# Performance work log

Measured on AMD Instinct MI355X. Metric: run time of the kernel, lower is better.

Reference implementation:

```python
import jax, jax.numpy as jnp
import numpy as np

N, L, D = 32, 4096, 768
H = 12
DH = D // H
MLP_DIM = 4 * D


def setup_inputs() -> dict:
    key = jax.random.key(0)
    ks = jax.random.split(key, 12)
    xavier = jax.nn.initializers.xavier_uniform()
    inp = {
        "x": jax.random.normal(ks[0], (N, L, D), jnp.float32),
        "probe": xavier(ks[1], (1, 1, D), jnp.float32),
        # MHA projections (flax DenseGeneral layout: (d, h, dh) / out (h, dh, d))
        "wq": xavier(ks[2], (D, H, DH), jnp.float32),
        "bq": jnp.zeros((H, DH), jnp.float32),
        "wk": xavier(ks[3], (D, H, DH), jnp.float32),
        "bk": jnp.zeros((H, DH), jnp.float32),
        "wv": xavier(ks[4], (D, H, DH), jnp.float32),
        "bv": jnp.zeros((H, DH), jnp.float32),
        "wo": xavier(ks[5], (H, DH, D), jnp.float32),
        "bo": jnp.zeros((D,), jnp.float32),
        # LayerNorm
        "ln_scale": jnp.ones((D,), jnp.float32),
        "ln_bias": jnp.zeros((D,), jnp.float32),
        # MLP block
        "w1": xavier(ks[6], (D, MLP_DIM), jnp.float32),
        "b1": jax.random.normal(ks[7], (MLP_DIM,), jnp.float32) * 1e-6,
        "w2": xavier(ks[8], (MLP_DIM, D), jnp.float32),
        "b2": jax.random.normal(ks[9], (D,), jnp.float32) * 1e-6,
    }
    return inp


def _layernorm(x, scale, bias, eps=1e-6):
    mu = jnp.mean(x, axis=-1, keepdims=True)
    var = jnp.mean(jnp.square(x - mu), axis=-1, keepdims=True)
    return (x - mu) * jax.lax.rsqrt(var + eps) * scale + bias


def reference(x, probe, wq, bq, wk, bk, wv, bv, wo, bo,
              ln_scale, ln_bias, w1, b1, w2, b2):
    n, l, d = x.shape
    q_in = jnp.broadcast_to(probe, (n, 1, d))          # tile probe over batch
    q = jnp.einsum('nqd,dhe->nqhe', q_in, wq) + bq     # [n,1,h,dh]
    k = jnp.einsum('nld,dhe->nlhe', x, wk) + bk        # [n,l,h,dh]
    v = jnp.einsum('nld,dhe->nlhe', x, wv) + bv
    q = q / jnp.sqrt(jnp.asarray(DH, q.dtype))
    logits = jnp.einsum('nqhe,nlhe->nhql', q, k)       # [n,h,1,l]
    attn = jax.nn.softmax(logits, axis=-1)
    o = jnp.einsum('nhql,nlhe->nqhe', attn, v)         # [n,1,h,dh]
    xa = jnp.einsum('nqhe,hed->nqd', o, wo) + bo       # attention output [n,1,d]
    y = _layernorm(xa, ln_scale, ln_bias)
    mlp = jnp.dot(jax.nn.gelu(jnp.dot(y, w1) + b1), w2) + b2
    out = xa + mlp
    return out[:, 0]                                   # [n,d]
```

## Files before the change

### kernel.cpp

```cpp
#include <hip/hip_runtime.h>
#include <math.h>

#define N_B 32
#define L_S 4096
#define D_M 768
#define H_N 12
#define NCH 16

#define ZO_QH    0
#define ZO_O     1024
#define ZO_XA    25600
#define ZO_H1P   50176
#define ZO_MACC  148480
#define ZERO_N   173056
#define NZ_QK    173056
#define NZ_QB    182272
#define NZ_MLC   182336
#define NZ_SLC   188480
#define NZ_SCL   194624
#define NZ_XBP   200768
#define NZ_Y     4919360

__global__ __launch_bounds__(256) void qh_kernel(
    const float* __restrict__ probe, const float* __restrict__ wq,
    const float* __restrict__ bq, float* __restrict__ qh) {
    int i = blockIdx.x * 256 + threadIdx.x;
    int d0 = blockIdx.y * 48;
    float acc = 0.f;
    for (int dd = 0; dd < 48; ++dd)
        acc += probe[d0 + dd] * wq[(size_t)(d0 + dd) * 768 + i];
    acc *= 0.125f;
    if (blockIdx.y == 0) acc += 0.125f * bq[i];
    atomicAdd(&qh[i], acc);
}

__global__ __launch_bounds__(256) void qk_kernel(
    const float* __restrict__ qh, const float* __restrict__ wk,
    const float* __restrict__ bk, float* __restrict__ qk,
    float* __restrict__ qb) {
    int h = blockIdx.x, dt = blockIdx.y, t = threadIdx.x;
    int d = dt * 256 + t;
    const float4* wk4 = (const float4*)(wk + (size_t)d * 768 + h * 64);
    const float4* qh4 = (const float4*)(qh + h * 64);
    float acc = 0.f;
    #pragma unroll
    for (int e4 = 0; e4 < 16; ++e4) {
        float4 w = wk4[e4], q = qh4[e4];
        acc += w.x * q.x + w.y * q.y + w.z * q.z + w.w * q.w;
    }
    qk[h * 768 + d] = acc;
    if (dt == 0 && t < 64) {
        float v = qh[h * 64 + t] * bk[h * 64 + t];
        #pragma unroll
        for (int off = 32; off > 0; off >>= 1) v += __shfl_xor(v, off);
        if (t == 0) qb[h] = v;
    }
}

__global__ __launch_bounds__(256) void attn_fused(
    const float* __restrict__ x, const float* __restrict__ qk,
    const float* __restrict__ qb, float* __restrict__ xbp,
    float* __restrict__ mlc, float* __restrict__ slc) {
    __shared__ __align__(16) float qk_s[12 * 772];
    __shared__ __align__(16) float xs[2 * 4 * 772];
    __shared__ float lg_s[64], w_s[64], qb_s[16], ms_s[16], ss_s[16], sc_s[16];
    int lc = blockIdx.x, n = blockIdx.y, t = threadIdx.x;
    int lane = t & 63, w = t >> 6;
    size_t xbase = ((size_t)n * 4096 + lc * 256) * 768;

    for (int i = t; i < 12 * 192; i += 256) {
        int hh = i / 192, c = i % 192;
        ((float4*)&qk_s[hh * 772])[c] = ((const float4*)qk)[i];
    }
    if (t < 12) { qb_s[t] = qb[t]; ms_s[t] = -1e30f; ss_s[t] = 0.f; }
    {
        const float4* s0 = (const float4*)(x + xbase);
        for (int j = t; j < 768; j += 256) {
            float4 v = s0[j];
            *((float4*)&xs[(j / 192) * 772 + (j % 192) * 4]) = v;
        }
    }
    float acc[12][3];
    #pragma unroll
    for (int h = 0; h < 12; ++h) { acc[h][0] = 0.f; acc[h][1] = 0.f; acc[h][2] = 0.f; }
    int q = t & 3, rh = t >> 2, h1 = rh % 12, r1 = t / 48;
    int d0 = t * 3;
    __syncthreads();

    int p = 0;
    for (int it = 0; it < 64; ++it) {
        if (w == 3 && it + 1 < 64) {
            const float4* src = (const float4*)(x + xbase + (size_t)(it + 1) * 3072);
            #pragma unroll
            for (int j = 0; j < 12; ++j) {
                int f = lane + 64 * j;
                float4 v = src[f];
                *((float4*)&xs[(p ^ 1) * 3088 + (f / 192) * 772 + (f % 192) * 4]) = v;
            }
        }
        if (t < 192) {
            const float4* xr = (const float4*)&xs[p * 3088 + r1 * 772];
            const float4* kr = (const float4*)&qk_s[h1 * 772];
            float a = 0.f;
            #pragma unroll 8
            for (int s = 0; s < 48; ++s) {
                int idx = s * 4 + q;
                float4 xv = xr[idx], kv = kr[idx];
                a += xv.x * kv.x + xv.y * kv.y + xv.z * kv.z + xv.w * kv.w;
            }
            a += __shfl_xor(a, 1);
            a += __shfl_xor(a, 2);
            if (q == 0) lg_s[r1 * 16 + h1] = a + qb_s[h1];
        }
        __syncthreads();
        if (t < 12) {
            float l0 = lg_s[0 * 16 + t], l1 = lg_s[1 * 16 + t];
            float l2 = lg_s[2 * 16 + t], l3 = lg_s[3 * 16 + t];
            float mt = fmaxf(fmaxf(l0, l1), fmaxf(l2, l3));
            float mo = ms_s[t];
            float mn = fmaxf(mo, mt);
            float sc = __expf(mo - mn);
            float e0 = __expf(l0 - mn), e1 = __expf(l1 - mn);
            float e2 = __expf(l2 - mn), e3 = __expf(l3 - mn);
            w_s[0 * 16 + t] = e0; w_s[1 * 16 + t] = e1;
            w_s[2 * 16 + t] = e2; w_s[3 * 16 + t] = e3;
            ms_s[t] = mn;
            ss_s[t] = ss_s[t] * sc + (e0 + e1 + e2 + e3);
            sc_s[t] = sc;
        }
        __syncthreads();
        const float* xb = &xs[p * 3088];
        #pragma unroll
        for (int h = 0; h < 12; ++h) {
            float sc = sc_s[h];
            acc[h][0] *= sc; acc[h][1] *= sc; acc[h][2] *= sc;
        }
        #pragma unroll
        for (int l = 0; l < 4; ++l) {
            float x0 = xb[l * 772 + d0], x1 = xb[l * 772 + d0 + 1], x2 = xb[l * 772 + d0 + 2];
            #pragma unroll
            for (int h = 0; h < 12; ++h) {
                float wv = w_s[l * 16 + h];
                acc[h][0] += wv * x0; acc[h][1] += wv * x1; acc[h][2] += wv * x2;
            }
        }
        __syncthreads();
        p ^= 1;
    }
    size_t ob = ((size_t)(lc * 32 + n)) * 12 * 768;
    #pragma unroll
    for (int h = 0; h < 12; ++h) {
        xbp[ob + h * 768 + d0 + 0] = acc[h][0];
        xbp[ob + h * 768 + d0 + 1] = acc[h][1];
        xbp[ob + h * 768 + d0 + 2] = acc[h][2];
    }
    if (t < 12) {
        mlc[(n * 12 + t) * 16 + lc] = ms_s[t];
        slc[(n * 12 + t) * 16 + lc] = ss_s[t];
    }
}

__global__ __launch_bounds__(256) void merge_kernel(
    const float* __restrict__ mlc, const float* __restrict__ slc,
    float* __restrict__ scl) {
    int t = threadIdx.x;
    for (int pr = t; pr < 384; pr += 256) {
        float M = -1e30f;
        #pragma unroll
        for (int c = 0; c < 16; ++c) M = fmaxf(M, mlc[pr * 16 + c]);
        float e[16];
        float T = 0.f;
        #pragma unroll
        for (int c = 0; c < 16; ++c) {
            e[c] = __expf(mlc[pr * 16 + c] - M);
            T += slc[pr * 16 + c] * e[c];
        }
        float inv = 1.f / T;
        int n = pr / 12, h = pr % 12;
        #pragma unroll
        for (int c = 0; c < 16; ++c)
            scl[(c * 32 + n) * 12 + h] = e[c] * inv;
    }
}

__global__ __launch_bounds__(256) void oproj_kernel(
    const float* __restrict__ xbp, const float* __restrict__ scl,
    const float* __restrict__ wv, const float* __restrict__ bv,
    float* __restrict__ o) {
    int h = blockIdx.x, kk = blockIdx.y, t = threadIdx.x;
    int d0 = kk * 96;
    __shared__ __align__(16) float wv_s[96 * 64];
    __shared__ __align__(16) float xb_s[96 * 32];
    for (int i = t; i < 96 * 64; i += 256) {
        int d = i >> 6, e = i & 63;
        wv_s[i] = wv[(size_t)(d0 + d) * 768 + h * 64 + e];
    }
    for (int i = t; i < 96 * 32; i += 256) {
        int d = i >> 5, nn = i & 31;
        float s = 0.f;
        #pragma unroll
        for (int lcc = 0; lcc < 16; ++lcc)
            s += xbp[(((size_t)lcc * 32 + nn) * 12 + h) * 768 + d0 + d]
               * scl[(lcc * 32 + nn) * 12 + h];
        xb_s[i] = s;
    }
    __syncthreads();
    int e = t & 63, ng = t >> 6;
    float acc[8] = {0, 0, 0, 0, 0, 0, 0, 0};
    for (int d = 0; d < 96; ++d) {
        float wvv = wv_s[d * 64 + e];
        const float4* xb4 = (const float4*)&xb_s[d * 32 + ng * 8];
        float4 p0 = xb4[0], p1 = xb4[1];
        acc[0] += p0.x * wvv; acc[1] += p0.y * wvv; acc[2] += p0.z * wvv; acc[3] += p0.w * wvv;
        acc[4] += p1.x * wvv; acc[5] += p1.y * wvv; acc[6] += p1.z * wvv; acc[7] += p1.w * wvv;
    }
    float bvv = (kk == 0) ? bv[h * 64 + e] : 0.f;
    #pragma unroll
    for (int k = 0; k < 8; ++k)
        atomicAdd(&o[(size_t)(ng * 8 + k) * 768 + h * 64 + e], acc[k] + bvv);
}

__global__ __launch_bounds__(256) void xaproj_kernel(
    const float* __restrict__ o, const float* __restrict__ wo,
    const float* __restrict__ bo, float* __restrict__ xa) {
    int dt = blockIdx.x, kk = blockIdx.y, t = threadIdx.x;
    int i0 = kk * 96;
    __shared__ __align__(16) float o_s[96 * 32];
    for (int idx = t; idx < 96 * 32; idx += 256) {
        int i = idx >> 5, nn = idx & 31;
        o_s[idx] = o[(size_t)nn * 768 + i0 + i];
    }
    __syncthreads();
    int d = dt * 256 + t;
    float acc[32];
    #pragma unroll
    for (int nn = 0; nn < 32; ++nn) acc[nn] = 0.f;
    for (int i = 0; i < 96; ++i) {
        float w = wo[(size_t)(i0 + i) * 768 + d];
        const float4* o4 = (const float4*)&o_s[i * 32];
        #pragma unroll
        for (int qq = 0; qq < 8; ++qq) {
            float4 f = o4[qq];
            acc[qq * 4 + 0] += f.x * w; acc[qq * 4 + 1] += f.y * w;
            acc[qq * 4 + 2] += f.z * w; acc[qq * 4 + 3] += f.w * w;
        }
    }
    float bov = (kk == 0) ? bo[d] : 0.f;
    #pragma unroll
    for (int nn = 0; nn < 32; ++nn)
        atomicAdd(&xa[(size_t)nn * 768 + d], acc[nn] + bov);
}

__global__ __launch_bounds__(256) void ln_kernel(
    const float* __restrict__ xa, const float* __restrict__ ln_scale,
    const float* __restrict__ ln_bias, float* __restrict__ y) {
    int n = blockIdx.x, tid = threadIdx.x;
    __shared__ float xs[768];
    __shared__ float red[4];
    for (int i = tid; i < 768; i += 256) xs[i] = xa[(size_t)n * 768 + i];
    __syncthreads();
    float lsum = 0.f;
    for (int i = tid; i < 768; i += 256) lsum += xs[i];
    #pragma unroll
    for (int off = 32; off > 0; off >>= 1) lsum += __shfl_xor(lsum, off);
    int wave = tid >> 6;
    if ((tid & 63) == 0) red[wave] = lsum;
    __syncthreads();
    float mu = (red[0] + red[1] + red[2] + red[3]) * (1.f / 768.f);
    __syncthreads();
    float lsq = 0.f;
    for (int i = tid; i < 768; i += 256) { float c = xs[i] - mu; lsq += c * c; }
    #pragma unroll
    for (int off = 32; off > 0; off >>= 1) lsq += __shfl_xor(lsq, off);
    if ((tid & 63) == 0) red[wave] = lsq;
    __syncthreads();
    float var = (red[0] + red[1] + red[2] + red[3]) * (1.f / 768.f);
    float rs = rsqrtf(var + 1e-6f);
    for (int i = tid; i < 768; i += 256)
        y[(size_t)n * 768 + i] = (xs[i] - mu) * rs * ln_scale[i] + ln_bias[i];
}

__global__ __launch_bounds__(256) void mlp1_kernel(
    const float* __restrict__ y, const float* __restrict__ w1,
    float* __restrict__ h1p) {
    int jt = blockIdx.x, kk = blockIdx.y, t = threadIdx.x;
    int d0 = kk * 48;
    __shared__ __align__(16) float y_s[48 * 32];
    for (int idx = t; idx < 48 * 32; idx += 256) {
        int d = idx >> 5, nn = idx & 31;
        y_s[idx] = y[(size_t)nn * 768 + d0 + d];
    }
    __syncthreads();
    int j = jt * 256 + t;
    float acc[32];
    #pragma unroll
    for (int nn = 0; nn < 32; ++nn) acc[nn] = 0.f;
    for (int d = 0; d < 48; ++d) {
        float w = w1[(size_t)(d0 + d) * 3072 + j];
        const float4* y4 = (const float4*)&y_s[d * 32];
        #pragma unroll
        for (int qq = 0; qq < 8; ++qq) {
            float4 f = y4[qq];
            acc[qq * 4 + 0] += f.x * w; acc[qq * 4 + 1] += f.y * w;
            acc[qq * 4 + 2] += f.z * w; acc[qq * 4 + 3] += f.w * w;
        }
    }
    #pragma unroll
    for (int nn = 0; nn < 32; ++nn)
        atomicAdd(&h1p[(size_t)nn * 3072 + j], acc[nn]);
}

__global__ __launch_bounds__(256) void mlp2_kernel(
    const float* __restrict__ h1p, const float* __restrict__ b1,
    const float* __restrict__ w2, float* __restrict__ macc) {
    int dt = blockIdx.x, kk = blockIdx.y, t = threadIdx.x;
    int j0 = kk * 48;
    __shared__ __align__(16) float h_s[48 * 32];
    for (int idx = t; idx < 48 * 32; idx += 256) {
        int j = idx >> 5, nn = idx & 31;
        float tv = h1p[(size_t)nn * 3072 + j0 + j] + b1[j0 + j];
        float u = 0.7978845608028654f * (tv + 0.044715f * tv * tv * tv);
        h_s[idx] = 0.5f * tv * (1.f + tanhf(u));
    }
    __syncthreads();
    int d = dt * 256 + t;
    float acc[32];
    #pragma unroll
    for (int nn = 0; nn < 32; ++nn) acc[nn] = 0.f;
    for (int j = 0; j < 48; ++j) {
        float w = w2[(size_t)(j0 + j) * 768 + d];
        const float4* h4 = (const float4*)&h_s[j * 32];
        #pragma unroll
        for (int qq = 0; qq < 8; ++qq) {
            float4 f = h4[qq];
            acc[qq * 4 + 0] += f.x * w; acc[qq * 4 + 1] += f.y * w;
            acc[qq * 4 + 2] += f.z * w; acc[qq * 4 + 3] += f.w * w;
        }
    }
    #pragma unroll
    for (int nn = 0; nn < 32; ++nn)
        atomicAdd(&macc[(size_t)nn * 768 + d], acc[nn]);
}

__global__ __launch_bounds__(256) void final_kernel(
    const float* __restrict__ xa, const float* __restrict__ b2,
    const float* __restrict__ macc, float* __restrict__ out) {
    int n = blockIdx.x, t = threadIdx.x;
    for (int i = t; i < 768; i += 256)
        out[(size_t)n * 768 + i] = xa[(size_t)n * 768 + i] + b2[i] + macc[(size_t)n * 768 + i];
}

extern "C" void kernel_launch(void* const* d_in, const int* in_sizes, int n_in,
                              void* d_out, int out_size, void* d_ws, size_t ws_size,
                              hipStream_t stream) {
    const float* x        = (const float*)d_in[0];
    const float* probe    = (const float*)d_in[1];
    const float* wq       = (const float*)d_in[2];
    const float* bq       = (const float*)d_in[3];
    const float* wk       = (const float*)d_in[4];
    const float* bk       = (const float*)d_in[5];
    const float* wv       = (const float*)d_in[6];
    const float* bv       = (const float*)d_in[7];
    const float* wo       = (const float*)d_in[8];
    const float* bo       = (const float*)d_in[9];
    const float* ln_scale = (const float*)d_in[10];
    const float* ln_bias  = (const float*)d_in[11];
    const float* w1       = (const float*)d_in[12];
    const float* b1       = (const float*)d_in[13];
    const float* w2       = (const float*)d_in[14];
    const float* b2       = (const float*)d_in[15];
    float* out = (float*)d_out;
    float* ws  = (float*)d_ws;

    float* qh   = ws + ZO_QH;
    float* o    = ws + ZO_O;
    float* xa   = ws + ZO_XA;
    float* h1p  = ws + ZO_H1P;
    float* macc = ws + ZO_MACC;
    float* qk   = ws + NZ_QK;
    float* qb   = ws + NZ_QB;
    float* mlc  = ws + NZ_MLC;
    float* slc  = ws + NZ_SLC;
    float* scl  = ws + NZ_SCL;
    float* xbp  = ws + NZ_XBP;
    float* y    = ws + NZ_Y;

    hipMemsetAsync(ws, 0, (size_t)ZERO_N * sizeof(float), stream);
    qh_kernel<<<dim3(3, 16), 256, 0, stream>>>(probe, wq, bq, qh);
    qk_kernel<<<dim3(12, 3), 256, 0, stream>>>(qh, wk, bk, qk, qb);
    attn_fused<<<dim3(NCH, 32), 256, 0, stream>>>(x, qk, qb, xbp, mlc, slc);
    merge_kernel<<<1, 256, 0, stream>>>(mlc, slc, scl);
    oproj_kernel<<<dim3(12, 8), 256, 0, stream>>>(xbp, scl, wv, bv, o);
    xaproj_kernel<<<dim3(3, 8), 256, 0, stream>>>(o, wo, bo, xa);
    ln_kernel<<<N_B, 256, 0, stream>>>(xa, ln_scale, ln_bias, y);
    mlp1_kernel<<<dim3(12, 16), 256, 0, stream>>>(y, w1, h1p);
    mlp2_kernel<<<dim3(3, 64), 256, 0, stream>>>(h1p, b1, w2, macc);
    final_kernel<<<N_B, 256, 0, stream>>>(xa, b2, macc, out);
}
```

Baseline: 759.4 us.

## Replace atomics with partial-sum buffers, fold merge kernel, vectorize attention accumulation

Every atomicAdd reduction (qh, o, xa, h1p, macc) is replaced by writes to per-split partial buffers that the next kernel sums, so the workspace memset is no longer needed. The softmax merge kernel is folded into oproj, removing one launch. The MLP kernels get fewer, larger K splits. In the attention kernel, 192 threads now each accumulate a float4 of 4 columns per head, with padding changed from 772 to 776. The cost is extra partial-buffer traffic, and the value-accumulation step now leaves a quarter of the threads idle.

Result: slower. 845.9 us (+11.4%).

```diff
diff --git a/kernel.cpp b/kernel.cpp
--- a/kernel.cpp
+++ b/kernel.cpp
@@ -6,42 +6,50 @@
 #define D_M 768
 #define H_N 12
 #define NCH 16
-
-#define ZO_QH    0
-#define ZO_O     1024
-#define ZO_XA    25600
-#define ZO_H1P   50176
-#define ZO_MACC  148480
-#define ZERO_N   173056
-#define NZ_QK    173056
-#define NZ_QB    182272
-#define NZ_MLC   182336
-#define NZ_SLC   188480
-#define NZ_SCL   194624
-#define NZ_XBP   200768
-#define NZ_Y     4919360
+#define XP  776
+
+#define WS_QHP    0
+#define WS_QK     12288
+#define WS_QB     21504
+#define WS_MLC    21568
+#define WS_SLC    27712
+#define WS_XBP    33856
+#define WS_OP     4752448
+#define WS_XAP    4949056
+#define WS_XAS    5145664
+#define WS_Y      5170240
+#define WS_H1P    5194816
+#define WS_MACCP  5588032
 
 __global__ __launch_bounds__(256) void qh_kernel(
     const float* __restrict__ probe, const float* __restrict__ wq,
-    const float* __restrict__ bq, float* __restrict__ qh) {
+    const float* __restrict__ bq, float* __restrict__ qhp) {
     int i = blockIdx.x * 256 + threadIdx.x;
-    int d0 = blockIdx.y * 48;
+    int ky = blockIdx.y, d0 = ky * 48;
     float acc = 0.f;
     for (int dd = 0; dd < 48; ++dd)
         acc += probe[d0 + dd] * wq[(size_t)(d0 + dd) * 768 + i];
     acc *= 0.125f;
-    if (blockIdx.y == 0) acc += 0.125f * bq[i];
-    atomicAdd(&qh[i], acc);
+    if (ky == 0) acc += 0.125f * bq[i];
+    qhp[ky * 768 + i] = acc;
 }
 
 __global__ __launch_bounds__(256) void qk_kernel(
-    const float* __restrict__ qh, const float* __restrict__ wk,
+    const float* __restrict__ qhp, const float* __restrict__ wk,
     const float* __restrict__ bk, float* __restrict__ qk,
     float* __restrict__ qb) {
     int h = blockIdx.x, dt = blockIdx.y, t = threadIdx.x;
+    __shared__ float qh_s[64];
+    if (t < 64) {
+        float s = 0.f;
+        #pragma unroll
+        for (int k = 0; k < 16; ++k) s += qhp[k * 768 + h * 64 + t];
+        qh_s[t] = s;
+    }
+    __syncthreads();
     int d = dt * 256 + t;
     const float4* wk4 = (const float4*)(wk + (size_t)d * 768 + h * 64);
-    const float4* qh4 = (const float4*)(qh + h * 64);
+    const float4* qh4 = (const float4*)qh_s;
     float acc = 0.f;
     #pragma unroll
     for (int e4 = 0; e4 < 16; ++e4) {
@@ -50,7 +58,7 @@
     }
     qk[h * 768 + d] = acc;
     if (dt == 0 && t < 64) {
-        float v = qh[h * 64 + t] * bk[h * 64 + t];
+        float v = qh_s[t] * bk[h * 64 + t];
         #pragma unroll
         for (int off = 32; off > 0; off >>= 1) v += __shfl_xor(v, off);
         if (t == 0) qb[h] = v;
@@ -61,8 +69,8 @@
     const float* __restrict__ x, const float* __restrict__ qk,
     const float* __restrict__ qb, float* __restrict__ xbp,
     float* __restrict__ mlc, float* __restrict__ slc) {
-    __shared__ __align__(16) float qk_s[12 * 772];
-    __shared__ __align__(16) float xs[2 * 4 * 772];
+    __shared__ __align__(16) float qk_s[12 * XP];
+    __shared__ __align__(16) float xs[2 * 4 * XP];
     __shared__ float lg_s[64], w_s[64], qb_s[16], ms_s[16], ss_s[16], sc_s[16];
     int lc = blockIdx.x, n = blockIdx.y, t = threadIdx.x;
     int lane = t & 63, w = t >> 6;
@@ -70,21 +78,18 @@
 
     for (int i = t; i < 12 * 192; i += 256) {
         int hh = i / 192, c = i % 192;
-        ((float4*)&qk_s[hh * 772])[c] = ((const float4*)qk)[i];
+        *(float4*)&qk_s[hh * XP + c * 4] = ((const float4*)qk)[i];
     }
     if (t < 12) { qb_s[t] = qb[t]; ms_s[t] = -1e30f; ss_s[t] = 0.f; }
     {
         const float4* s0 = (const float4*)(x + xbase);
-        for (int j = t; j < 768; j += 256) {
-            float4 v = s0[j];
-            *((float4*)&xs[(j / 192) * 772 + (j % 192) * 4]) = v;
-        }
-    }
-    float acc[12][3];
-    #pragma unroll
-    for (int h = 0; h < 12; ++h) { acc[h][0] = 0.f; acc[h][1] = 0.f; acc[h][2] = 0.f; }
-    int q = t & 3, rh = t >> 2, h1 = rh % 12, r1 = t / 48;
-    int d0 = t * 3;
+        for (int j = t; j < 768; j += 256)
+            *(float4*)&xs[(j / 192) * XP + (j % 192) * 4] = s0[j];
+    }
+    float4 acc4[12];
+    #pragma unroll
+    for (int h = 0; h < 12; ++h) acc4[h] = make_float4(0.f, 0.f, 0.f, 0.f);
+    int r1 = t & 3, q1 = (t >> 2) & 3, h1 = t >> 4;
     __syncthreads();
 
     int p = 0;
@@ -95,22 +100,22 @@
             for (int j = 0; j < 12; ++j) {
                 int f = lane + 64 * j;
                 float4 v = src[f];
-                *((float4*)&xs[(p ^ 1) * 3088 + (f / 192) * 772 + (f % 192) * 4]) = v;
+                *(float4*)&xs[(p ^ 1) * 4 * XP + (f / 192) * XP + (f % 192) * 4] = v;
             }
         }
         if (t < 192) {
-            const float4* xr = (const float4*)&xs[p * 3088 + r1 * 772];
-            const float4* kr = (const float4*)&qk_s[h1 * 772];
+            const float4* xr = (const float4*)&xs[p * 4 * XP + r1 * XP];
+            const float4* kr = (const float4*)&qk_s[h1 * XP];
             float a = 0.f;
             #pragma unroll 8
             for (int s = 0; s < 48; ++s) {
-                int idx = s * 4 + q;
+                int idx = s * 4 + q1;
                 float4 xv = xr[idx], kv = kr[idx];
                 a += xv.x * kv.x + xv.y * kv.y + xv.z * kv.z + xv.w * kv.w;
             }
-            a += __shfl_xor(a, 1);
-            a += __shfl_xor(a, 2);
-            if (q == 0) lg_s[r1 * 16 + h1] = a + qb_s[h1];
+            a += __shfl_xor(a, 4);
+            a += __shfl_xor(a, 8);
+            if (q1 == 0) lg_s[r1 * 16 + h1] = a + qb_s[h1];
         }
         __syncthreads();
         if (t < 12) {
@@ -129,30 +134,49 @@
             sc_s[t] = sc;
         }
         __syncthreads();
-        const float* xb = &xs[p * 3088];
-        #pragma unroll
-        for (int h = 0; h < 12; ++h) {
-            float sc = sc_s[h];
-            acc[h][0] *= sc; acc[h][1] *= sc; acc[h][2] *= sc;
-        }
-        #pragma unroll
-        for (int l = 0; l < 4; ++l) {
-            float x0 = xb[l * 772 + d0], x1 = xb[l * 772 + d0 + 1], x2 = xb[l * 772 + d0 + 2];
+        if (t < 192) {
+            const float* xb = &xs[p * 4 * XP];
+            const float4* w4 = (const float4*)w_s;
+            const float4* sc4 = (const float4*)sc_s;
+            float4 sa = sc4[0], sb = sc4[1], sc = sc4[2];
+            acc4[0].x *= sa.x; acc4[0].y *= sa.x; acc4[0].z *= sa.x; acc4[0].w *= sa.x;
+            acc4[1].x *= sa.y; acc4[1].y *= sa.y; acc4[1].z *= sa.y; acc4[1].w *= sa.y;
+            acc4[2].x *= sa.z; acc4[2].y *= sa.z; acc4[2].z *= sa.z; acc4[2].w *= sa.z;
+            acc4[3].x *= sa.w; acc4[3].y *= sa.w; acc4[3].z *= sa.w; acc4[3].w *= sa.w;
+            acc4[4].x *= sb.x; acc4[4].y *= sb.x; acc4[4].z *= sb.x; acc4[4].w *= sb.x;
+            acc4[5].x *= sb.y; acc4[5].y *= sb.y; acc4[5].z *= sb.y; acc4[5].w *= sb.y;
+            acc4[6].x *= sb.z; acc4[6].y *= sb.z; acc4[6].z *= sb.z; acc4[6].w *= sb.z;
+            acc4[7].x *= sb.w; acc4[7].y *= sb.w; acc4[7].z *= sb.w; acc4[7].w *= sb.w;
+            acc4[8].x *= sc.x; acc4[8].y *= sc.x; acc4[8].z *= sc.x; acc4[8].w *= sc.x;
+            acc4[9].x *= sc.y; acc4[9].y *= sc.y; acc4[9].z *= sc.y; acc4[9].w *= sc.y;
+            acc4[10].x *= sc.z; acc4[10].y *= sc.z; acc4[10].z *= sc.z; acc4[10].w *= sc.z;
+            acc4[11].x *= sc.w; acc4[11].y *= sc.w; acc4[11].z *= sc.w; acc4[11].w *= sc.w;
             #pragma unroll
-            for (int h = 0; h < 12; ++h) {
-                float wv = w_s[l * 16 + h];
-                acc[h][0] += wv * x0; acc[h][1] += wv * x1; acc[h][2] += wv * x2;
+            for (int l = 0; l < 4; ++l) {
+                float4 xv = *(const float4*)&xb[l * XP + 4 * t];
+                float4 wa = w4[l * 4], wb = w4[l * 4 + 1], wc = w4[l * 4 + 2];
+                acc4[0].x += wa.x * xv.x; acc4[0].y += wa.x * xv.y; acc4[0].z += wa.x * xv.z; acc4[0].w += wa.x * xv.w;
+                acc4[1].x += wa.y * xv.x; acc4[1].y += wa.y * xv.y; acc4[1].z += wa.y * xv.z; acc4[1].w += wa.y * xv.w;
+                acc4[2].x += wa.z * xv.x; acc4[2].y += wa.z * xv.y; acc4[2].z += wa.z * xv.z; acc4[2].w += wa.z * xv.w;
+                acc4[3].x += wa.w * xv.x; acc4[3].y += wa.w * xv.y; acc4[3].z += wa.w * xv.z; acc4[3].w += wa.w * xv.w;
+                acc4[4].x += wb.x * xv.x; acc4[4].y += wb.x * xv.y; acc4[4].z += wb.x * xv.z; acc4[4].w += wb.x * xv.w;
+                acc4[5].x += wb.y * xv.x; acc4[5].y += wb.y * xv.y; acc4[5].z += wb.y * xv.z; acc4[5].w += wb.y * xv.w;
+                acc4[6].x += wb.z * xv.x; acc4[6].y += wb.z * xv.y; acc4[6].z += wb.z * xv.z; acc4[6].w += wb.z * xv.w;
+                acc4[7].x += wb.w * xv.x; acc4[7].y += wb.w * xv.y; acc4[7].z += wb.w * xv.z; acc4[7].w += wb.w * xv.w;
+                acc4[8].x += wc.x * xv.x; acc4[8].y += wc.x * xv.y; acc4[8].z += wc.x * xv.z; acc4[8].w += wc.x * xv.w;
+                acc4[9].x += wc.y * xv.x; acc4[9].y += wc.y * xv.y; acc4[9].z += wc.y * xv.z; acc4[9].w += wc.y * xv.w;
+                acc4[10].x += wc.z * xv.x; acc4[10].y += wc.z * xv.y; acc4[10].z += wc.z * xv.z; acc4[10].w += wc.z * xv.w;
+                acc4[11].x += wc.w * xv.x; acc4[11].y += wc.w * xv.y; acc4[11].z += wc.w * xv.z; acc4[11].w += wc.w * xv.w;
             }
         }
         __syncthreads();
         p ^= 1;
     }
     size_t ob = ((size_t)(lc * 32 + n)) * 12 * 768;
-    #pragma unroll
-    for (int h = 0; h < 12; ++h) {
-        xbp[ob + h * 768 + d0 + 0] = acc[h][0];
-        xbp[ob + h * 768 + d0 + 1] = acc[h][1];
-        xbp[ob + h * 768 + d0 + 2] = acc[h][2];
+    if (t < 192) {
+        #pragma unroll
+        for (int h = 0; h < 12; ++h)
+            *(float4*)&xbp[ob + h * 768 + 4 * t] = acc4[h];
     }
     if (t < 12) {
         mlc[(n * 12 + t) * 16 + lc] = ms_s[t];
@@ -160,48 +184,41 @@
     }
 }
 
-__global__ __launch_bounds__(256) void merge_kernel(
-    const float* __restrict__ mlc, const float* __restrict__ slc,
-    float* __restrict__ scl) {
-    int t = threadIdx.x;
-    for (int pr = t; pr < 384; pr += 256) {
-        float M = -1e30f;
-        #pragma unroll
-        for (int c = 0; c < 16; ++c) M = fmaxf(M, mlc[pr * 16 + c]);
-        float e[16];
-        float T = 0.f;
-        #pragma unroll
-        for (int c = 0; c < 16; ++c) {
-            e[c] = __expf(mlc[pr * 16 + c] - M);
-            T += slc[pr * 16 + c] * e[c];
-        }
-        float inv = 1.f / T;
-        int n = pr / 12, h = pr % 12;
-        #pragma unroll
-        for (int c = 0; c < 16; ++c)
-            scl[(c * 32 + n) * 12 + h] = e[c] * inv;
-    }
-}
-
 __global__ __launch_bounds__(256) void oproj_kernel(
-    const float* __restrict__ xbp, const float* __restrict__ scl,
-    const float* __restrict__ wv, const float* __restrict__ bv,
-    float* __restrict__ o) {
+    const float* __restrict__ xbp, const float* __restrict__ mlc,
+    const float* __restrict__ slc, const float* __restrict__ wv,
+    const float* __restrict__ bv, float* __restrict__ op) {
     int h = blockIdx.x, kk = blockIdx.y, t = threadIdx.x;
     int d0 = kk * 96;
     __shared__ __align__(16) float wv_s[96 * 64];
     __shared__ __align__(16) float xb_s[96 * 32];
+    __shared__ float scl_s[16 * 32];
+    if (t < 32) {
+        float M = -1e30f;
+        #pragma unroll
+        for (int c = 0; c < 16; ++c) M = fmaxf(M, mlc[(t * 12 + h) * 16 + c]);
+        float e[16], T = 0.f;
+        #pragma unroll
+        for (int c = 0; c < 16; ++c) {
+            e[c] = __expf(mlc[(t * 12 + h) * 16 + c] - M);
+            T += slc[(t * 12 + h) * 16 + c] * e[c];
+        }
+        float inv = 1.f / T;
+        #pragma unroll
+        for (int c = 0; c < 16; ++c) scl_s[c * 32 + t] = e[c] * inv;
+    }
     for (int i = t; i < 96 * 64; i += 256) {
         int d = i >> 6, e = i & 63;
         wv_s[i] = wv[(size_t)(d0 + d) * 768 + h * 64 + e];
     }
+    __syncthreads();
     for (int i = t; i < 96 * 32; i += 256) {
         int d = i >> 5, nn = i & 31;
         float s = 0.f;
         #pragma unroll
         for (int lcc = 0; lcc < 16; ++lcc)
             s += xbp[(((size_t)lcc * 32 + nn) * 12 + h) * 768 + d0 + d]
-               * scl[(lcc * 32 + nn) * 12 + h];
+               * scl_s[lcc * 32 + nn];
         xb_s[i] = s;
     }
     __syncthreads();
@@ -217,18 +234,22 @@
     float bvv = (kk == 0) ? bv[h * 64 + e] : 0.f;
     #pragma unroll
     for (int k = 0; k < 8; ++k)
-        atomicAdd(&o[(size_t)(ng * 8 + k) * 768 + h * 64 + e], acc[k] + bvv);
+        op[(size_t)kk * 24576 + (size_t)(ng * 8 + k) * 768 + h * 64 + e] = acc[k] + bvv;
 }
 
 __global__ __launch_bounds__(256) void xaproj_kernel(
-    const float* __restrict__ o, const float* __restrict__ wo,
-    const float* __restrict__ bo, float* __restrict__ xa) {
+    const float* __restrict__ op, const float* __restrict__ wo,
+    const float* __restrict__ bo, float* __restrict__ xap) {
     int dt = blockIdx.x, kk = blockIdx.y, t = threadIdx.x;
     int i0 = kk * 96;
     __shared__ __align__(16) float o_s[96 * 32];
     for (int idx = t; idx < 96 * 32; idx += 256) {
         int i = idx >> 5, nn = idx & 31;
-        o_s[idx] = o[(size_t)nn * 768 + i0 + i];
+        float s = 0.f;
+        #pragma unroll
+        for (int pp = 0; pp < 8; ++pp)
+            s += op[(size_t)pp * 24576 + (size_t)nn * 768 + i0 + i];
+        o_s[idx] = s;
     }
     __syncthreads();
     int d = dt * 256 + t;
@@ -248,16 +269,24 @@
     float bov = (kk == 0) ? bo[d] : 0.f;
     #pragma unroll
     for (int nn = 0; nn < 32; ++nn)
-        atomicAdd(&xa[(size_t)nn * 768 + d], acc[nn] + bov);
+        xap[(size_t)kk * 24576 + (size_t)nn * 768 + d] = acc[nn] + bov;
 }
 
 __global__ __launch_bounds__(256) void ln_kernel(
-    const float* __restrict__ xa, const float* __restrict__ ln_scale,
-    const float* __restrict__ ln_bias, float* __restrict__ y) {
+    const float* __restrict__ xap, const float* __restrict__ ln_scale,
+    const float* __restrict__ ln_bias, float* __restrict__ xas,
+    float* __restrict__ y) {
     int n = blockIdx.x, tid = threadIdx.x;
     __shared__ float xs[768];
     __shared__ float red[4];
-    for (int i = tid; i < 768; i += 256) xs[i] = xa[(size_t)n * 768 + i];
+    for (int i = tid; i < 768; i += 256) {
+        float s = 0.f;
+        #pragma unroll
+        for (int pp = 0; pp < 8; ++pp)
+            s += xap[(size_t)pp * 24576 + (size_t)n * 768 + i];
+        xs[i] = s;
+        xas[(size_t)n * 768 + i] = s;
+    }
     __syncthreads();
     float lsum = 0.f;
     for (int i = tid; i < 768; i += 256) lsum += xs[i];
@@ -284,9 +313,9 @@
     const float* __restrict__ y, const float* __restrict__ w1,
     float* __restrict__ h1p) {
     int jt = blockIdx.x, kk = blockIdx.y, t = threadIdx.x;
-    int d0 = kk * 48;
-    __shared__ __align__(16) float y_s[48 * 32];
-    for (int idx = t; idx < 48 * 32; idx += 256) {
+    int d0 = kk * 192;
+    __shared__ __align__(16) float y_s[192 * 32];
+    for (int idx = t; idx < 192 * 32; idx += 256) {
         int d = idx >> 5, nn = idx & 31;
         y_s[idx] = y[(size_t)nn * 768 + d0 + d];
     }
@@ -295,7 +324,7 @@
     float acc[32];
     #pragma unroll
     for (int nn = 0; nn < 32; ++nn) acc[nn] = 0.f;
-    for (int d = 0; d < 48; ++d) {
+    for (int d = 0; d < 192; ++d) {
         float w = w1[(size_t)(d0 + d) * 3072 + j];
         const float4* y4 = (const float4*)&y_s[d * 32];
         #pragma unroll
@@ -307,18 +336,21 @@
     }
     #pragma unroll
     for (int nn = 0; nn < 32; ++nn)
-        atomicAdd(&h1p[(size_t)nn * 3072 + j], acc[nn]);
+        h1p[(size_t)kk * 98304 + (size_t)nn * 3072 + j] = acc[nn];
 }
 
 __global__ __launch_bounds__(256) void mlp2_kernel(
     const float* __restrict__ h1p, const float* __restrict__ b1,
-    const float* __restrict__ w2, float* __restrict__ macc) {
+    const float* __restrict__ w2, float* __restrict__ maccp) {
     int dt = blockIdx.x, kk = blockIdx.y, t = threadIdx.x;
-    int j0 = kk * 48;
-    __shared__ __align__(16) float h_s[48 * 32];
-    for (int idx = t; idx < 48 * 32; idx += 256) {
+    int j0 = kk * 192;
+    __shared__ __align__(16) float h_s[192 * 32];
+    for (int idx = t; idx < 192 * 32; idx += 256) {
         int j = idx >> 5, nn = idx & 31;
-        float tv = h1p[(size_t)nn * 3072 + j0 + j] + b1[j0 + j];
+        float tv = b1[j0 + j];
+        #pragma unroll
+        for (int pp = 0; pp < 4; ++pp)
+            tv += h1p[(size_t)pp * 98304 + (size_t)nn * 3072 + j0 + j];
         float u = 0.7978845608028654f * (tv + 0.044715f * tv * tv * tv);
         h_s[idx] = 0.5f * tv * (1.f + tanhf(u));
     }
@@ -327,7 +359,7 @@
     float acc[32];
     #pragma unroll
     for (int nn = 0; nn < 32; ++nn) acc[nn] = 0.f;
-    for (int j = 0; j < 48; ++j) {
+    for (int j = 0; j < 192; ++j) {
         float w = w2[(size_t)(j0 + j) * 768 + d];
         const float4* h4 = (const float4*)&h_s[j * 32];
         #pragma unroll
@@ -339,15 +371,20 @@
     }
     #pragma unroll
     for (int nn = 0; nn < 32; ++nn)
-        atomicAdd(&macc[(size_t)nn * 768 + d], acc[nn]);
+        maccp[(size_t)kk * 24576 + (size_t)nn * 768 + d] = acc[nn];
 }
 
 __global__ __launch_bounds__(256) void final_kernel(
-    const float* __restrict__ xa, const float* __restrict__ b2,
-    const float* __restrict__ macc, float* __restrict__ out) {
+    const float* __restrict__ xas, const float* __restrict__ b2,
+    const float* __restrict__ maccp, float* __restrict__ out) {
     int n = blockIdx.x, t = threadIdx.x;
-    for (int i = t; i < 768; i += 256)
-        out[(size_t)n * 768 + i] = xa[(size_t)n * 768 + i] + b2[i] + macc[(size_t)n * 768 + i];
+    for (int i = t; i < 768; i += 256) {
+        float s = xas[(size_t)n * 768 + i] + b2[i];
+        #pragma unroll
+        for (int k = 0; k < 16; ++k)
+            s += maccp[(size_t)k * 24576 + (size_t)n * 768 + i];
+        out[(size_t)n * 768 + i] = s;
+    }
 }
 
 extern "C" void kernel_launch(void* const* d_in, const int* in_sizes, int n_in,
@@ -372,28 +409,26 @@
     float* out = (float*)d_out;
     float* ws  = (float*)d_ws;
 
-    float* qh   = ws + ZO_QH;
-    float* o    = ws + ZO_O;
-    float* xa   = ws + ZO_XA;
-    float* h1p  = ws + ZO_H1P;
-    float* macc = ws + ZO_MACC;
-    float* qk   = ws + NZ_QK;
-    float* qb   = ws + NZ_QB;
-    float* mlc  = ws + NZ_MLC;
-    float* slc  = ws + NZ_SLC;
-    float* scl  = ws + NZ_SCL;
-    float* xbp  = ws + NZ_XBP;
-    float* y    = ws + NZ_Y;
-
-    hipMemsetAsync(ws, 0, (size_t)ZERO_N * sizeof(float), stream);
-    qh_kernel<<<dim3(3, 16), 256, 0, stream>>>(probe, wq, bq, qh);
-    qk_kernel<<<dim3(12, 3), 256, 0, stream>>>(qh, wk, bk, qk, qb);
+    float* qhp   = ws + WS_QHP;
+    float* qk    = ws + WS_QK;
+    float* qb    = ws + WS_QB;
+    float* mlc   = ws + WS_MLC;
+    float* slc   = ws + WS_SLC;
+    float* xbp   = ws + WS_XBP;
+    float* op    = ws + WS_OP;
+    float* xap   = ws + WS_XAP;
+    float* xas   = ws + WS_XAS;
+    float* y     = ws + WS_Y;
+    float* h1p   = ws + WS_H1P;
+    float* maccp = ws + WS_MACCP;
+
+    qh_kernel<<<dim3(3, 16), 256, 0, stream>>>(probe, wq, bq, qhp);
+    qk_kernel<<<dim3(12, 3), 256, 0, stream>>>(qhp, wk, bk, qk, qb);
     attn_fused<<<dim3(NCH, 32), 256, 0, stream>>>(x, qk, qb, xbp, mlc, slc);
-    merge_kernel<<<1, 256, 0, stream>>>(mlc, slc, scl);
-    oproj_kernel<<<dim3(12, 8), 256, 0, stream>>>(xbp, scl, wv, bv, o);
-    xaproj_kernel<<<dim3(3, 8), 256, 0, stream>>>(o, wo, bo, xa);
-    ln_kernel<<<N_B, 256, 0, stream>>>(xa, ln_scale, ln_bias, y);
-    mlp1_kernel<<<dim3(12, 16), 256, 0, stream>>>(y, w1, h1p);
-    mlp2_kernel<<<dim3(3, 64), 256, 0, stream>>>(h1p, b1, w2, macc);
-    final_kernel<<<N_B, 256, 0, stream>>>(xa, b2, macc, out);
-}
+    oproj_kernel<<<dim3(12, 8), 256, 0, stream>>>(xbp, mlc, slc, wv, bv, op);
+    xaproj_kernel<<<dim3(3, 8), 256, 0, stream>>>(op, wo, bo, xap);
+    ln_kernel<<<N_B, 256, 0, stream>>>(xap, ln_scale, ln_bias, xas, y);
+    mlp1_kernel<<<dim3(12, 4), 256, 0, stream>>>(y, w1, h1p);
+    mlp2_kernel<<<dim3(3, 16), 256, 0, stream>>>(h1p, b1, w2, maccp);
+    final_kernel<<<N_B, 256, 0, stream>>>(xas, b2, maccp, out);
+}
```
